# Kernel tuning notes

Hardware: AMD Instinct MI355X
Metric: run time of the kernel (lower is better)

## Reference

```python
import jax, jax.numpy as jnp
import numpy as np

HIDDEN, MSG, KEY, ROUNDS = 256, 64, 16, 2
LN_EPS = 1e-5


def _orthogonal(key, shape, gain):
    # mimic torch orthogonal_ init (exact values don't matter for correctness testing)
    a = jax.random.normal(key, shape, dtype=jnp.float32)
    q, r = jnp.linalg.qr(a.T if shape[0] < shape[1] else a)
    q = q * jnp.sign(jnp.diag(r))
    if shape[0] < shape[1]:
        q = q.T
    return gain * q[:shape[0], :shape[1]]


def setup_inputs() -> dict:
    key = jax.random.key(0)
    ks = jax.random.split(key, 6)
    g = float(np.sqrt(2.0))
    N = 8192
    return {
        "hidden_states": jax.random.normal(ks[0], (N, HIDDEN), dtype=jnp.float32),
        "W_msg": _orthogonal(ks[1], (MSG, HIDDEN), g),
        "b_msg": jnp.zeros((MSG,), jnp.float32),
        "W_key": _orthogonal(ks[2], (KEY, HIDDEN), g),
        "b_key": jnp.zeros((KEY,), jnp.float32),
        "W_qry": _orthogonal(ks[3], (KEY, HIDDEN), g),
        "b_qry": jnp.zeros((KEY,), jnp.float32),
        "W_agg": _orthogonal(ks[4], (HIDDEN, HIDDEN + MSG), g),
        "b_agg": jnp.zeros((HIDDEN,), jnp.float32),
        "ln_g": jnp.ones((HIDDEN,), jnp.float32),
        "ln_b": jnp.zeros((HIDDEN,), jnp.float32),
    }


def reference(hidden_states, W_msg, b_msg, W_key, b_key, W_qry, b_qry,
              W_agg, b_agg, ln_g, ln_b):
    inv_sqrt_k = 1.0 / np.sqrt(KEY)
    h = hidden_states
    attn = None
    for _ in range(ROUNDS):
        msgs = h @ W_msg.T + b_msg          # (N, MSG)
        keys = h @ W_key.T + b_key          # (N, KEY)
        qrys = h @ W_qry.T + b_qry          # (N, KEY)
        scores = (qrys @ keys.T) * inv_sqrt_k  # (N, N)
        attn = jax.nn.softmax(scores, axis=-1)
        agg_msg = attn @ msgs               # (N, MSG)
        combined = jnp.concatenate([h, agg_msg], axis=-1)  # (N, HIDDEN+MSG)
        z = combined @ W_agg.T + b_agg      # (N, HIDDEN)
        mu = jnp.mean(z, axis=-1, keepdims=True)
        var = jnp.mean(jnp.square(z - mu), axis=-1, keepdims=True)
        h = jax.nn.relu(ln_g * (z - mu) * jax.lax.rsqrt(var + LN_EPS) + ln_b)
    return h, attn
```

## Files before the change

kernel.cpp:

```cpp
#include <hip/hip_runtime.h>

constexpr int H = 256, MSGC = 64;
constexpr float LN_EPS = 1e-5f;
constexpr float QSCALE = 0.25f * 1.4426950408889634f;

typedef __attribute__((ext_vector_type(8))) short bf16x8;
typedef __attribute__((ext_vector_type(4))) float f32x4;

__device__ inline ushort f2bf(float x) {
    union { float f; unsigned u; } v; v.f = x;
    unsigned r = v.u + 0x7fffu + ((v.u >> 16) & 1u);
    return (ushort)(r >> 16);
}
__device__ inline float bf2f(ushort h) {
    union { unsigned u; float f; } v; v.u = ((unsigned)h) << 16;
    return v.f;
}
__device__ inline bf16x8 pack_bf16x8(float4 f0, float4 f1) {
    union { unsigned u[4]; bf16x8 v; } cv;
    asm("v_cvt_pk_bf16_f32 %0, %1, %2" : "=v"(cv.u[0]) : "v"(f0.x), "v"(f0.y));
    asm("v_cvt_pk_bf16_f32 %0, %1, %2" : "=v"(cv.u[1]) : "v"(f0.z), "v"(f0.w));
    asm("v_cvt_pk_bf16_f32 %0, %1, %2" : "=v"(cv.u[2]) : "v"(f1.x), "v"(f1.y));
    asm("v_cvt_pk_bf16_f32 %0, %1, %2" : "=v"(cv.u[3]) : "v"(f1.z), "v"(f1.w));
    return cv.v;
}

__global__ __launch_bounds__(256) void prep_kernel(
    const float* __restrict__ Wm, const float* __restrict__ Wk,
    const float* __restrict__ Wq, const float* __restrict__ Wa,
    ushort* __restrict__ Wph, ushort* __restrict__ Wpl,
    ushort* __restrict__ Wfh, ushort* __restrict__ Wfl)
{
    const int t = threadIdx.x, b = blockIdx.x;
    if (b < 48) {
        const int tile = b >> 3, kc = b & 7;
#pragma unroll
        for (int j2 = 0; j2 < 2; ++j2) {
            const int idx = t * 2 + j2;
            const int l = idx >> 3, e = idx & 7;
            const int col = tile * 16 + (l & 15);
            const int k = kc * 32 + (l >> 4) * 8 + e;
            float v;
            if (col < 64)      v = Wm[(size_t)col * H + k];
            else if (col < 80) v = Wk[(size_t)(col - 64) * H + k];
            else               v = QSCALE * Wq[(size_t)(col - 80) * H + k];
            ushort hi = f2bf(v);
            Wph[(size_t)b * 512 + idx] = hi;
            Wpl[(size_t)b * 512 + idx] = f2bf(v - bf2f(hi));
        }
    } else {
        const int unit = b - 48;
        const int ctg = unit / 10, kc = unit % 10;
#pragma unroll
        for (int j2 = 0; j2 < 2; ++j2) {
            const int idx = t * 2 + j2;
            const int l = idx >> 3, e = idx & 7;
            const int col = ctg * 16 + (l & 15);
            const int k = kc * 32 + (l >> 4) * 8 + e;
            const float v = Wa[(size_t)col * 320 + k];
            ushort hi = f2bf(v);
            Wfh[(size_t)unit * 512 + idx] = hi;
            Wfl[(size_t)unit * 512 + idx] = f2bf(v - bf2f(hi));
        }
    }
}

__global__ __launch_bounds__(128) void proj_kernel(
    const float* __restrict__ h,
    const ushort* __restrict__ Wph, const ushort* __restrict__ Wpl,
    const float* __restrict__ bm, const float* __restrict__ bk, const float* __restrict__ bq,
    ushort* __restrict__ msgsF, ushort* __restrict__ kh, ushort* __restrict__ kl,
    ushort* __restrict__ qh, ushort* __restrict__ ql, int n)
{
    constexpr int AST = 264;
    __shared__ ushort Ahi[16 * AST];
    __shared__ ushort Alo[16 * AST];
    const int t = threadIdx.x, lane = t & 63, w = t >> 6;
    const int gq = lane >> 4, c = lane & 15;
    const int r0 = blockIdx.x * 16;
    const float4* hsrc = (const float4*)(h + (size_t)r0 * H);
#pragma unroll
    for (int u = 0; u < 8; ++u) {
        const int idx = t + 128 * u;
        const int row = idx >> 6, c4 = idx & 63;
        float4 v = hsrc[idx];
        ushort4 hi, lo;
        hi.x = f2bf(v.x); lo.x = f2bf(v.x - bf2f(hi.x));
        hi.y = f2bf(v.y); lo.y = f2bf(v.y - bf2f(hi.y));
        hi.z = f2bf(v.z); lo.z = f2bf(v.z - bf2f(hi.z));
        hi.w = f2bf(v.w); lo.w = f2bf(v.w - bf2f(hi.w));
        *(ushort4*)&Ahi[row * AST + c4 * 4] = hi;
        *(ushort4*)&Alo[row * AST + c4 * 4] = lo;
    }
    __syncthreads();
    f32x4 acc[3] = {{0,0,0,0},{0,0,0,0},{0,0,0,0}};
    for (int kc = 0; kc < 8; ++kc) {
        const bf16x8 afh = *(const bf16x8*)&Ahi[c * AST + kc * 32 + gq * 8];
        const bf16x8 afl = *(const bf16x8*)&Alo[c * AST + kc * 32 + gq * 8];
#pragma unroll
        for (int ct = 0; ct < 3; ++ct) {
            const int unit = (w * 3 + ct) * 8 + kc;
            const bf16x8 whi = *(const bf16x8*)(Wph + (size_t)unit * 512 + lane * 8);
            const bf16x8 wlo = *(const bf16x8*)(Wpl + (size_t)unit * 512 + lane * 8);
            acc[ct] = __builtin_amdgcn_mfma_f32_16x16x32_bf16(afh, whi, acc[ct], 0, 0, 0);
            acc[ct] = __builtin_amdgcn_mfma_f32_16x16x32_bf16(afh, wlo, acc[ct], 0, 0, 0);
            acc[ct] = __builtin_amdgcn_mfma_f32_16x16x32_bf16(afl, whi, acc[ct], 0, 0, 0);
        }
    }
#pragma unroll
    for (int ct = 0; ct < 3; ++ct) {
        const int tile = w * 3 + ct;
        if (tile < 4) {
            const float bb = bm[tile * 16 + c];
#pragma unroll
            for (int r = 0; r < 4; ++r) {
                const int j = r0 + gq * 4 + r;
                const size_t idx = ((size_t)(j >> 5) * 4 + tile) * 512
                                 + ((j >> 3) & 3) * 128 + c * 8 + (j & 7);
                msgsF[idx] = f2bf(acc[ct][r] + bb);
            }
        } else if (tile == 4) {
            const float bb = bk[c];
#pragma unroll
            for (int r = 0; r < 4; ++r) {
                const int j = r0 + gq * 4 + r;
                const float v = acc[ct][r] + bb;
                const ushort hi = f2bf(v);
                kh[(size_t)j * 16 + c] = hi;
                kl[(size_t)j * 16 + c] = f2bf(v - bf2f(hi));
            }
        } else {
            const float bb = QSCALE * bq[c];
#pragma unroll
            for (int r = 0; r < 4; ++r) {
                const int j = r0 + gq * 4 + r;
                const float v = acc[ct][r] + bb;
                const ushort hi = f2bf(v);
                qh[(size_t)j * 16 + c] = hi;
                ql[(size_t)j * 16 + c] = f2bf(v - bf2f(hi));
            }
        }
    }
}

__device__ __forceinline__ void loadK(bf16x8* dst, const ushort* __restrict__ kh,
                                      int j0, int g, int c) {
#pragma unroll
    for (int js = 0; js < 4; ++js)
        dst[js] = *(const bf16x8*)(kh + (size_t)(j0 + js * 16 + c) * 16 + 8 * (g & 1));
}

__device__ __forceinline__ void qk_tile(const bf16x8* b1s, const ushort* __restrict__ kl,
                                        int j0, int g, int c, bf16x8 a1, bf16x8 a2,
                                        const bf16x8 zer, f32x4* pd) {
    const f32x4 z4 = {0.f, 0.f, 0.f, 0.f};
    bf16x8 b2s[4];
#pragma unroll
    for (int js = 0; js < 4; ++js)
        b2s[js] = (g < 2) ? *(const bf16x8*)(kl + (size_t)(j0 + js * 16 + c) * 16 + 8 * g) : zer;
#pragma unroll
    for (int js = 0; js < 4; ++js) {
        pd[js] = __builtin_amdgcn_mfma_f32_16x16x32_bf16(a1, b1s[js], z4, 0, 0, 0);
        pd[js] = __builtin_amdgcn_mfma_f32_16x16x32_bf16(a2, b2s[js], pd[js], 0, 0, 0);
    }
}

__device__ __forceinline__ void pv_tile(const float* __restrict__ P,
                                        const ushort* __restrict__ msgsF,
                                        int j0, int g, int c, int w, int lane, f32x4* accv) {
#pragma unroll
    for (int ks = 0; ks < 2; ++ks) {
        const int arow = w * 16 + c;
        const int sw = (arow & 7) << 2;
        const int colb = ks * 32 + 8 * g;
        float4 f0 = *(const float4*)&P[arow * 64 + ((colb) ^ sw)];
        float4 f1 = *(const float4*)&P[arow * 64 + ((colb + 4) ^ sw)];
        bf16x8 af = pack_bf16x8(f0, f1);
        const size_t mbase = ((size_t)(j0 >> 5) + ks) * 4;
#pragma unroll
        for (int mt = 0; mt < 4; ++mt) {
            bf16x8 bfr = *((const bf16x8*)(msgsF + (mbase + mt) * 512) + lane);
            accv[mt] = __builtin_amdgcn_mfma_f32_16x16x32_bf16(af, bfr, accv[mt], 0, 0, 0);
        }
    }
}

__device__ __forceinline__ void expstore(const f32x4* pd, float* Pbuf, float* l,
                                         int w, int g, int c) {
#pragma unroll
    for (int js = 0; js < 4; ++js)
#pragma unroll
        for (int r = 0; r < 4; ++r) {
            const int row = w * 16 + g * 4 + r;
            const float pp = exp2f(pd[js][r]);
            l[r] += pp;
            Pbuf[row * 64 + ((js * 16 + c) ^ ((row & 7) << 2))] = pp;
        }
}

__device__ __forceinline__ void expstore_n(const f32x4* pd, float* Pbuf, const float* rinv,
                                           int w, int g, int c) {
#pragma unroll
    for (int js = 0; js < 4; ++js)
#pragma unroll
        for (int r = 0; r < 4; ++r) {
            const int row = w * 16 + g * 4 + r;
            const float pp = exp2f(pd[js][r]) * rinv[r];
            Pbuf[row * 64 + ((js * 16 + c) ^ ((row & 7) << 2))] = pp;
        }
}

__device__ __forceinline__ void attn_write(const float* __restrict__ Pbuf,
                                           float* __restrict__ attn,
                                           int i0, int j0, int n, int lane, int w) {
    const int c4 = lane & 15;
#pragma unroll
    for (int u = 0; u < 4; ++u) {
        const int row = w * 16 + u * 4 + (lane >> 4);
        const int sw = (row & 7) << 2;
        float4 v = *(const float4*)&Pbuf[row * 64 + ((c4 * 4) ^ sw)];
        *(float4*)(attn + (size_t)(i0 + row) * n + j0 + c4 * 4) = v;
    }
}

__global__ __launch_bounds__(256, 4) void flash1_kernel(
    const ushort* __restrict__ qh, const ushort* __restrict__ ql,
    const ushort* __restrict__ kh, const ushort* __restrict__ kl,
    const ushort* __restrict__ msgsF,
    float* __restrict__ aggO, float* __restrict__ aggL, int n)
{
    __shared__ float P0[64 * 64];
    __shared__ float P1[64 * 64];
    const int t = threadIdx.x, lane = t & 63, w = t >> 6;
    const int g = lane >> 4, c = lane & 15;
    const int i0 = blockIdx.x * 64;
    bf16x8 zer = {0,0,0,0,0,0,0,0};
    f32x4 z4 = {0.f, 0.f, 0.f, 0.f};
    const ushort* qsrc = (g < 2) ? qh : ql;
    bf16x8 a1 = *(const bf16x8*)(qsrc + (size_t)(i0 + w * 16 + c) * 16 + 8 * (g & 1));
    bf16x8 a2 = (g < 2) ? a1 : zer;
    float l[4] = {0.f, 0.f, 0.f, 0.f};
    f32x4 accv[4] = {z4, z4, z4, z4};
    const int nj = n / 8, jb = blockIdx.y * nj;
    bf16x8 bA[4], bB[4];
    loadK(bA, kh, jb, g, c);
    loadK(bB, kh, jb + 64, g, c);
    {
        f32x4 pd[4];
        qk_tile(bA, kl, jb, g, c, a1, a2, zer, pd);
        expstore(pd, P0, l, w, g, c);
    }
    loadK(bA, kh, jb + 128, g, c);
    {
        f32x4 pd[4];
        qk_tile(bB, kl, jb + 64, g, c, a1, a2, zer, pd);
        pv_tile(P0, msgsF, jb, g, c, w, lane, accv);
        expstore(pd, P1, l, w, g, c);
    }
    for (int p = 1; p < 8; ++p) {
        const int tA = jb + p * 128, tB = tA + 64;
        loadK(bB, kh, tB, g, c);
        {
            f32x4 pd[4];
            qk_tile(bA, kl, tA, g, c, a1, a2, zer, pd);
            pv_tile(P1, msgsF, tA - 64, g, c, w, lane, accv);
            expstore(pd, P0, l, w, g, c);
        }
        loadK(bA, kh, (p < 7) ? tA + 128 : tB, g, c);
        {
            f32x4 pd[4];
            qk_tile(bB, kl, tB, g, c, a1, a2, zer, pd);
            pv_tile(P0, msgsF, tA, g, c, w, lane, accv);
            expstore(pd, P1, l, w, g, c);
        }
    }
    pv_tile(P1, msgsF, jb + nj - 64, g, c, w, lane, accv);
#pragma unroll
    for (int r = 0; r < 4; ++r)
#pragma unroll
        for (int d2 = 1; d2 < 16; d2 <<= 1) l[r] += __shfl_xor(l[r], d2, 64);
#pragma unroll
    for (int mt = 0; mt < 4; ++mt)
#pragma unroll
        for (int r = 0; r < 4; ++r)
            aggO[((size_t)blockIdx.y * n + i0 + w * 16 + g * 4 + r) * MSGC + mt * 16 + c] = accv[mt][r];
    if (c == 0) {
#pragma unroll
        for (int r = 0; r < 4; ++r)
            aggL[(size_t)blockIdx.y * n + i0 + w * 16 + g * 4 + r] = l[r];
    }
}

__global__ __launch_bounds__(256, 4) void stats_kernel(
    const ushort* __restrict__ qh, const ushort* __restrict__ ql,
    const ushort* __restrict__ kh, const ushort* __restrict__ kl,
    float* __restrict__ rowl_p, int n)
{
    const int t = threadIdx.x, lane = t & 63, w = t >> 6;
    const int g = lane >> 4, c = lane & 15;
    const int iq = blockIdx.x * 64 + w * 16 + c;
    bf16x8 zer = {0,0,0,0,0,0,0,0};
    const ushort* qsrc = (g < 2) ? qh : ql;
    bf16x8 a1 = *(const bf16x8*)(qsrc + (size_t)iq * 16 + 8 * (g & 1));
    bf16x8 a2 = (g < 2) ? a1 : zer;
    const int nj = n / 8, jb = blockIdx.y * nj;
    float l[4] = {0.f, 0.f, 0.f, 0.f};
    bf16x8 bA[4], bB[4];
    loadK(bA, kh, jb, g, c);
    for (int p = 0; p < 8; ++p) {
        const int t0 = jb + p * 128, t1 = t0 + 64;
        const int t2 = (p < 7) ? t0 + 128 : t1;
        loadK(bB, kh, t1, g, c);
        {
            f32x4 pd[4];
            qk_tile(bA, kl, t0, g, c, a1, a2, zer, pd);
#pragma unroll
            for (int js = 0; js < 4; ++js)
#pragma unroll
                for (int r = 0; r < 4; ++r) l[r] += exp2f(pd[js][r]);
        }
        loadK(bA, kh, t2, g, c);
        {
            f32x4 pd[4];
            qk_tile(bB, kl, t1, g, c, a1, a2, zer, pd);
#pragma unroll
            for (int js = 0; js < 4; ++js)
#pragma unroll
                for (int r = 0; r < 4; ++r) l[r] += exp2f(pd[js][r]);
        }
    }
#pragma unroll
    for (int r = 0; r < 4; ++r)
#pragma unroll
        for (int d2 = 1; d2 < 16; d2 <<= 1) l[r] += __shfl_xor(l[r], d2, 64);
    if (c == 0) {
        const int q0 = blockIdx.x * 64 + w * 16 + g * 4;
#pragma unroll
        for (int r = 0; r < 4; ++r)
            rowl_p[(size_t)blockIdx.y * n + q0 + r] = l[r];
    }
}

__global__ __launch_bounds__(256, 4) void pass2_kernel(
    const ushort* __restrict__ qh, const ushort* __restrict__ ql,
    const ushort* __restrict__ kh, const ushort* __restrict__ kl,
    const ushort* __restrict__ msgsF, const float* __restrict__ rowl_p,
    float* __restrict__ aggO, float* __restrict__ attn, int n)
{
    __shared__ float P0[64 * 64];
    __shared__ float P1[64 * 64];
    const int t = threadIdx.x, lane = t & 63, w = t >> 6;
    const int g = lane >> 4, c = lane & 15;
    const int i0 = blockIdx.x * 64;
    bf16x8 zer = {0,0,0,0,0,0,0,0};
    f32x4 z4 = {0.f, 0.f, 0.f, 0.f};
    const ushort* qsrc = (g < 2) ? qh : ql;
    bf16x8 a1 = *(const bf16x8*)(qsrc + (size_t)(i0 + w * 16 + c) * 16 + 8 * (g & 1));
    bf16x8 a2 = (g < 2) ? a1 : zer;
    float rinv[4];
#pragma unroll
    for (int r = 0; r < 4; ++r) {
        const int q = i0 + w * 16 + g * 4 + r;
        float L = 0.f;
#pragma unroll
        for (int p = 0; p < 8; ++p) L += rowl_p[(size_t)p * n + q];
        rinv[r] = 1.f / L;
    }
    f32x4 accv[4] = {z4, z4, z4, z4};
    const int nj = n / 8, jb = blockIdx.y * nj;
    bf16x8 bA[4], bB[4];
    loadK(bA, kh, jb, g, c);
    loadK(bB, kh, jb + 64, g, c);
    {
        f32x4 pd[4];
        qk_tile(bA, kl, jb, g, c, a1, a2, zer, pd);
        expstore_n(pd, P0, rinv, w, g, c);
    }
    loadK(bA, kh, jb + 128, g, c);
    {
        f32x4 pd[4];
        qk_tile(bB, kl, jb + 64, g, c, a1, a2, zer, pd);
        attn_write(P0, attn, i0, jb, n, lane, w);
        pv_tile(P0, msgsF, jb, g, c, w, lane, accv);
        expstore_n(pd, P1, rinv, w, g, c);
    }
    for (int p = 1; p < 8; ++p) {
        const int tA = jb + p * 128, tB = tA + 64;
        loadK(bB, kh, tB, g, c);
        {
            f32x4 pd[4];
            qk_tile(bA, kl, tA, g, c, a1, a2, zer, pd);
            attn_write(P1, attn, i0, tA - 64, n, lane, w);
            pv_tile(P1, msgsF, tA - 64, g, c, w, lane, accv);
            expstore_n(pd, P0, rinv, w, g, c);
        }
        loadK(bA, kh, (p < 7) ? tA + 128 : tB, g, c);
        {
            f32x4 pd[4];
            qk_tile(bB, kl, tB, g, c, a1, a2, zer, pd);
            attn_write(P0, attn, i0, tA, n, lane, w);
            pv_tile(P0, msgsF, tA, g, c, w, lane, accv);
            expstore_n(pd, P1, rinv, w, g, c);
        }
    }
    attn_write(P1, attn, i0, jb + nj - 64, n, lane, w);
    pv_tile(P1, msgsF, jb + nj - 64, g, c, w, lane, accv);
#pragma unroll
    for (int mt = 0; mt < 4; ++mt)
#pragma unroll
        for (int r = 0; r < 4; ++r) {
            const int row = w * 16 + g * 4 + r;
            aggO[((size_t)blockIdx.y * n + i0 + row) * MSGC + mt * 16 + c] = accv[mt][r];
        }
}

template <bool FLASH>
__global__ __launch_bounds__(256) void aggln_kernel(
    const float* __restrict__ h, const float* __restrict__ aggO,
    const float* __restrict__ aggL,
    const ushort* __restrict__ Wfh, const ushort* __restrict__ Wfl,
    const float* __restrict__ ba,
    const float* __restrict__ gg, const float* __restrict__ bb,
    float* __restrict__ hout, int n)
{
    constexpr int AST = 328;
    __shared__ ushort Ahi[16 * AST];
    __shared__ ushort Alo[16 * AST];
    __shared__ float Linv[16];
    __shared__ float red1[16][4], red2[16][4];
    const int t = threadIdx.x, lane = t & 63, w = t >> 6;
    const int gq = lane >> 4, c = lane & 15;
    const int r0 = blockIdx.x * 16;
    const float4* hsrc = (const float4*)(h + (size_t)r0 * H);
#pragma unroll
    for (int u = 0; u < 4; ++u) {
        const int idx = t + 256 * u;
        const int row = idx >> 6, c4 = idx & 63;
        float4 v = hsrc[idx];
        ushort4 hi, lo;
        hi.x = f2bf(v.x); lo.x = f2bf(v.x - bf2f(hi.x));
        hi.y = f2bf(v.y); lo.y = f2bf(v.y - bf2f(hi.y));
        hi.z = f2bf(v.z); lo.z = f2bf(v.z - bf2f(hi.z));
        hi.w = f2bf(v.w); lo.w = f2bf(v.w - bf2f(hi.w));
        *(ushort4*)&Ahi[row * AST + c4 * 4] = hi;
        *(ushort4*)&Alo[row * AST + c4 * 4] = lo;
    }
    if (FLASH && t < 16) {
        float L = 0.f;
#pragma unroll
        for (int p = 0; p < 8; ++p) L += aggL[(size_t)p * n + r0 + t];
        Linv[t] = 1.f / L;
    }
    __syncthreads();
    {
        const int row = t >> 4, c4 = t & 15;
        float4 s = {0.f, 0.f, 0.f, 0.f};
#pragma unroll
        for (int p = 0; p < 8; ++p) {
            const float4 v = *(const float4*)(aggO + (size_t)p * n * MSGC
                               + (size_t)(r0 + row) * MSGC + c4 * 4);
            s.x += v.x; s.y += v.y; s.z += v.z; s.w += v.w;
        }
        if (FLASH) { const float li = Linv[row]; s.x *= li; s.y *= li; s.z *= li; s.w *= li; }
        ushort4 hi, lo;
        hi.x = f2bf(s.x); lo.x = f2bf(s.x - bf2f(hi.x));
        hi.y = f2bf(s.y); lo.y = f2bf(s.y - bf2f(hi.y));
        hi.z = f2bf(s.z); lo.z = f2bf(s.z - bf2f(hi.z));
        hi.w = f2bf(s.w); lo.w = f2bf(s.w - bf2f(hi.w));
        *(ushort4*)&Ahi[row * AST + 256 + c4 * 4] = hi;
        *(ushort4*)&Alo[row * AST + 256 + c4 * 4] = lo;
    }
    __syncthreads();
    f32x4 acc[4] = {{0,0,0,0},{0,0,0,0},{0,0,0,0},{0,0,0,0}};
    for (int kc = 0; kc < 10; ++kc) {
        const bf16x8 afh = *(const bf16x8*)&Ahi[c * AST + kc * 32 + gq * 8];
        const bf16x8 afl = *(const bf16x8*)&Alo[c * AST + kc * 32 + gq * 8];
#pragma unroll
        for (int ct = 0; ct < 4; ++ct) {
            const int ctg = w * 4 + ct;
            const bf16x8 whi = *(const bf16x8*)(Wfh + ((size_t)(ctg * 10 + kc)) * 512 + lane * 8);
            const bf16x8 wlo = *(const bf16x8*)(Wfl + ((size_t)(ctg * 10 + kc)) * 512 + lane * 8);
            acc[ct] = __builtin_amdgcn_mfma_f32_16x16x32_bf16(afh, whi, acc[ct], 0, 0, 0);
            acc[ct] = __builtin_amdgcn_mfma_f32_16x16x32_bf16(afh, wlo, acc[ct], 0, 0, 0);
            acc[ct] = __builtin_amdgcn_mfma_f32_16x16x32_bf16(afl, whi, acc[ct], 0, 0, 0);
        }
    }
    float bav[4], gv[4], bv[4];
#pragma unroll
    for (int ct = 0; ct < 4; ++ct) {
        const int col = w * 64 + ct * 16 + c;
        bav[ct] = ba[col]; gv[ct] = gg[col]; bv[ct] = bb[col];
    }
#pragma unroll
    for (int ct = 0; ct < 4; ++ct) {
        acc[ct][0] += bav[ct]; acc[ct][1] += bav[ct];
        acc[ct][2] += bav[ct]; acc[ct][3] += bav[ct];
    }
#pragma unroll
    for (int r = 0; r < 4; ++r) {
        float s1 = 0.f, s2 = 0.f;
#pragma unroll
        for (int ct = 0; ct < 4; ++ct) { const float v = acc[ct][r]; s1 += v; s2 += v * v; }
#pragma unroll
        for (int d = 1; d < 16; d <<= 1) { s1 += __shfl_xor(s1, d, 64); s2 += __shfl_xor(s2, d, 64); }
        if (c == 0) { red1[gq * 4 + r][w] = s1; red2[gq * 4 + r][w] = s2; }
    }
    __syncthreads();
#pragma unroll
    for (int r = 0; r < 4; ++r) {
        const int row = gq * 4 + r;
        const float s1 = red1[row][0] + red1[row][1] + red1[row][2] + red1[row][3];
        const float s2 = red2[row][0] + red2[row][1] + red2[row][2] + red2[row][3];
        const float mu = s1 * (1.f / 256.f);
        const float var = s2 * (1.f / 256.f) - mu * mu;
        const float rs = rsqrtf(var + LN_EPS);
#pragma unroll
        for (int ct = 0; ct < 4; ++ct) {
            float o = (acc[ct][r] - mu) * rs * gv[ct] + bv[ct];
            hout[(size_t)(r0 + row) * H + w * 64 + ct * 16 + c] = fmaxf(o, 0.f);
        }
    }
}

extern "C" void kernel_launch(void* const* d_in, const int* in_sizes, int n_in,
                              void* d_out, int out_size, void* d_ws, size_t ws_size,
                              hipStream_t stream)
{
    const float* hs = (const float*)d_in[0];
    const float* Wm = (const float*)d_in[1];
    const float* bm = (const float*)d_in[2];
    const float* Wk = (const float*)d_in[3];
    const float* bk = (const float*)d_in[4];
    const float* Wq = (const float*)d_in[5];
    const float* bq = (const float*)d_in[6];
    const float* Wa = (const float*)d_in[7];
    const float* ba = (const float*)d_in[8];
    const float* lg = (const float*)d_in[9];
    const float* lb = (const float*)d_in[10];
    const int n = in_sizes[0] / H;

    char* wp = (char*)d_ws;
    auto alloc = [&](size_t bytes) { void* p = (void*)wp; wp += (bytes + 255) & ~(size_t)255; return p; };
    float*  h2     = (float*)alloc((size_t)n * H * 4);
    ushort* qh     = (ushort*)alloc((size_t)n * 16 * 2);
    ushort* ql     = (ushort*)alloc((size_t)n * 16 * 2);
    ushort* kh     = (ushort*)alloc((size_t)n * 16 * 2);
    ushort* kl     = (ushort*)alloc((size_t)n * 16 * 2);
    ushort* msgsF  = (ushort*)alloc((size_t)MSGC * n * 2);
    float*  rowl_p = (float*)alloc((size_t)8 * n * 4);
    float*  aggO   = (float*)alloc((size_t)8 * n * MSGC * 4);
    float*  aggL   = (float*)alloc((size_t)8 * n * 4);
    ushort* Wph    = (ushort*)alloc((size_t)48 * 512 * 2);
    ushort* Wpl    = (ushort*)alloc((size_t)48 * 512 * 2);
    ushort* Wfh    = (ushort*)alloc((size_t)160 * 512 * 2);
    ushort* Wfl    = (ushort*)alloc((size_t)160 * 512 * 2);

    float* hOut = (float*)d_out;
    float* attn = hOut + (size_t)n * H;

    prep_kernel<<<208, 256, 0, stream>>>(Wm, Wk, Wq, Wa, Wph, Wpl, Wfh, Wfl);

    proj_kernel<<<n / 16, 128, 0, stream>>>(hs, Wph, Wpl, bm, bk, bq, msgsF, kh, kl, qh, ql, n);
    flash1_kernel<<<dim3(n / 64, 8), 256, 0, stream>>>(qh, ql, kh, kl, msgsF,
                                                       aggO, aggL, n);
    aggln_kernel<true><<<n / 16, 256, 0, stream>>>(hs, aggO, aggL, Wfh, Wfl,
                                                   ba, lg, lb, h2, n);
    proj_kernel<<<n / 16, 128, 0, stream>>>(h2, Wph, Wpl, bm, bk, bq, msgsF, kh, kl, qh, ql, n);
    stats_kernel<<<dim3(n / 64, 8), 256, 0, stream>>>(qh, ql, kh, kl, rowl_p, n);
    pass2_kernel<<<dim3(n / 64, 8), 256, 0, stream>>>(qh, ql, kh, kl, msgsF,
                                                      rowl_p, aggO, attn, n);
    aggln_kernel<false><<<n / 16, 256, 0, stream>>>(h2, aggO, aggL, Wfh, Wfl,
                                                    ba, lg, lb, hOut, n);
}
```

Before: 244.5 us.

## Use native exp2, MFMA priority hints, higher occupancy bounds, 8-row aggln blocks

```diff
diff --git a/kernel.cpp b/kernel.cpp
--- a/kernel.cpp
+++ b/kernel.cpp
@@ -6,6 +6,12 @@
 
 typedef __attribute__((ext_vector_type(8))) short bf16x8;
 typedef __attribute__((ext_vector_type(4))) float f32x4;
+
+#if __has_builtin(__builtin_amdgcn_exp2f)
+__device__ __forceinline__ float fexp2(float x) { return __builtin_amdgcn_exp2f(x); }
+#else
+__device__ __forceinline__ float fexp2(float x) { return exp2f(x); }
+#endif
 
 __device__ inline ushort f2bf(float x) {
     union { float f; unsigned u; } v; v.f = x;
@@ -16,12 +22,17 @@
     union { unsigned u; float f; } v; v.u = ((unsigned)h) << 16;
     return v.f;
 }
+__device__ inline unsigned cvt_pk_u32(float a, float b) {
+    unsigned r;
+    asm("v_cvt_pk_bf16_f32 %0, %1, %2" : "=v"(r) : "v"(a), "v"(b));
+    return r;
+}
 __device__ inline bf16x8 pack_bf16x8(float4 f0, float4 f1) {
     union { unsigned u[4]; bf16x8 v; } cv;
-    asm("v_cvt_pk_bf16_f32 %0, %1, %2" : "=v"(cv.u[0]) : "v"(f0.x), "v"(f0.y));
-    asm("v_cvt_pk_bf16_f32 %0, %1, %2" : "=v"(cv.u[1]) : "v"(f0.z), "v"(f0.w));
-    asm("v_cvt_pk_bf16_f32 %0, %1, %2" : "=v"(cv.u[2]) : "v"(f1.x), "v"(f1.y));
-    asm("v_cvt_pk_bf16_f32 %0, %1, %2" : "=v"(cv.u[3]) : "v"(f1.z), "v"(f1.w));
+    cv.u[0] = cvt_pk_u32(f0.x, f0.y);
+    cv.u[1] = cvt_pk_u32(f0.z, f0.w);
+    cv.u[2] = cvt_pk_u32(f1.x, f1.y);
+    cv.u[3] = cvt_pk_u32(f1.z, f1.w);
     return cv.v;
 }
 
@@ -158,11 +169,13 @@
 #pragma unroll
     for (int js = 0; js < 4; ++js)
         b2s[js] = (g < 2) ? *(const bf16x8*)(kl + (size_t)(j0 + js * 16 + c) * 16 + 8 * g) : zer;
+    __builtin_amdgcn_s_setprio(1);
 #pragma unroll
     for (int js = 0; js < 4; ++js) {
         pd[js] = __builtin_amdgcn_mfma_f32_16x16x32_bf16(a1, b1s[js], z4, 0, 0, 0);
         pd[js] = __builtin_amdgcn_mfma_f32_16x16x32_bf16(a2, b2s[js], pd[js], 0, 0, 0);
     }
+    __builtin_amdgcn_s_setprio(0);
 }
 
 __device__ __forceinline__ void pv_tile(const float* __restrict__ P,
@@ -177,11 +190,13 @@
         float4 f1 = *(const float4*)&P[arow * 64 + ((colb + 4) ^ sw)];
         bf16x8 af = pack_bf16x8(f0, f1);
         const size_t mbase = ((size_t)(j0 >> 5) + ks) * 4;
+        __builtin_amdgcn_s_setprio(1);
 #pragma unroll
         for (int mt = 0; mt < 4; ++mt) {
             bf16x8 bfr = *((const bf16x8*)(msgsF + (mbase + mt) * 512) + lane);
             accv[mt] = __builtin_amdgcn_mfma_f32_16x16x32_bf16(af, bfr, accv[mt], 0, 0, 0);
         }
+        __builtin_amdgcn_s_setprio(0);
     }
 }
 
@@ -192,7 +207,7 @@
 #pragma unroll
         for (int r = 0; r < 4; ++r) {
             const int row = w * 16 + g * 4 + r;
-            const float pp = exp2f(pd[js][r]);
+            const float pp = fexp2(pd[js][r]);
             l[r] += pp;
             Pbuf[row * 64 + ((js * 16 + c) ^ ((row & 7) << 2))] = pp;
         }
@@ -205,14 +220,14 @@
 #pragma unroll
         for (int r = 0; r < 4; ++r) {
             const int row = w * 16 + g * 4 + r;
-            const float pp = exp2f(pd[js][r]) * rinv[r];
+            const float pp = fexp2(pd[js][r]) * rinv[r];
             Pbuf[row * 64 + ((js * 16 + c) ^ ((row & 7) << 2))] = pp;
         }
 }
 
-__device__ __forceinline__ void attn_write(const float* __restrict__ Pbuf,
-                                           float* __restrict__ attn,
-                                           int i0, int j0, int n, int lane, int w) {
+__device__ __forceinline__ void attn_write4(const float* __restrict__ Pbuf,
+                                            float* __restrict__ attn,
+                                            int i0, int j0, int n, int lane, int w) {
     const int c4 = lane & 15;
 #pragma unroll
     for (int u = 0; u < 4; ++u) {
@@ -223,7 +238,7 @@
     }
 }
 
-__global__ __launch_bounds__(256, 4) void flash1_kernel(
+__global__ __launch_bounds__(256, 5) void flash1_kernel(
     const ushort* __restrict__ qh, const ushort* __restrict__ ql,
     const ushort* __restrict__ kh, const ushort* __restrict__ kl,
     const ushort* __restrict__ msgsF,
@@ -291,7 +306,7 @@
     }
 }
 
-__global__ __launch_bounds__(256, 4) void stats_kernel(
+__global__ __launch_bounds__(256, 6) void stats_kernel(
     const ushort* __restrict__ qh, const ushort* __restrict__ ql,
     const ushort* __restrict__ kh, const ushort* __restrict__ kl,
     float* __restrict__ rowl_p, int n)
@@ -317,7 +332,7 @@
 #pragma unroll
             for (int js = 0; js < 4; ++js)
 #pragma unroll
-                for (int r = 0; r < 4; ++r) l[r] += exp2f(pd[js][r]);
+                for (int r = 0; r < 4; ++r) l[r] += fexp2(pd[js][r]);
         }
         loadK(bA, kh, t2, g, c);
         {
@@ -326,7 +341,7 @@
 #pragma unroll
             for (int js = 0; js < 4; ++js)
 #pragma unroll
-                for (int r = 0; r < 4; ++r) l[r] += exp2f(pd[js][r]);
+                for (int r = 0; r < 4; ++r) l[r] += fexp2(pd[js][r]);
         }
     }
 #pragma unroll
@@ -341,7 +356,7 @@
     }
 }
 
-__global__ __launch_bounds__(256, 4) void pass2_kernel(
+__global__ __launch_bounds__(256, 5) void pass2_kernel(
     const ushort* __restrict__ qh, const ushort* __restrict__ ql,
     const ushort* __restrict__ kh, const ushort* __restrict__ kl,
     const ushort* __restrict__ msgsF, const float* __restrict__ rowl_p,
@@ -380,7 +395,7 @@
     {
         f32x4 pd[4];
         qk_tile(bB, kl, jb + 64, g, c, a1, a2, zer, pd);
-        attn_write(P0, attn, i0, jb, n, lane, w);
+        attn_write4(P0, attn, i0, jb, n, lane, w);
         pv_tile(P0, msgsF, jb, g, c, w, lane, accv);
         expstore_n(pd, P1, rinv, w, g, c);
     }
@@ -390,7 +405,7 @@
         {
             f32x4 pd[4];
             qk_tile(bA, kl, tA, g, c, a1, a2, zer, pd);
-            attn_write(P1, attn, i0, tA - 64, n, lane, w);
+            attn_write4(P1, attn, i0, tA - 64, n, lane, w);
             pv_tile(P1, msgsF, tA - 64, g, c, w, lane, accv);
             expstore_n(pd, P0, rinv, w, g, c);
         }
@@ -398,12 +413,12 @@
         {
             f32x4 pd[4];
             qk_tile(bB, kl, tB, g, c, a1, a2, zer, pd);
-            attn_write(P0, attn, i0, tA, n, lane, w);
+            attn_write4(P0, attn, i0, tA, n, lane, w);
             pv_tile(P0, msgsF, tA, g, c, w, lane, accv);
             expstore_n(pd, P1, rinv, w, g, c);
         }
     }
-    attn_write(P1, attn, i0, jb + nj - 64, n, lane, w);
+    attn_write4(P1, attn, i0, jb + nj - 64, n, lane, w);
     pv_tile(P1, msgsF, jb + nj - 64, g, c, w, lane, accv);
 #pragma unroll
     for (int mt = 0; mt < 4; ++mt)
@@ -426,17 +441,17 @@
     constexpr int AST = 328;
     __shared__ ushort Ahi[16 * AST];
     __shared__ ushort Alo[16 * AST];
-    __shared__ float Linv[16];
+    __shared__ float Linv[8];
     __shared__ float red1[16][4], red2[16][4];
     const int t = threadIdx.x, lane = t & 63, w = t >> 6;
     const int gq = lane >> 4, c = lane & 15;
-    const int r0 = blockIdx.x * 16;
+    const int r0 = blockIdx.x * 8;
     const float4* hsrc = (const float4*)(h + (size_t)r0 * H);
 #pragma unroll
     for (int u = 0; u < 4; ++u) {
         const int idx = t + 256 * u;
         const int row = idx >> 6, c4 = idx & 63;
-        float4 v = hsrc[idx];
+        float4 v = (row < 8) ? hsrc[idx] : make_float4(0.f, 0.f, 0.f, 0.f);
         ushort4 hi, lo;
         hi.x = f2bf(v.x); lo.x = f2bf(v.x - bf2f(hi.x));
         hi.y = f2bf(v.y); lo.y = f2bf(v.y - bf2f(hi.y));
@@ -445,14 +460,14 @@
         *(ushort4*)&Ahi[row * AST + c4 * 4] = hi;
         *(ushort4*)&Alo[row * AST + c4 * 4] = lo;
     }
-    if (FLASH && t < 16) {
+    if (FLASH && t < 8) {
         float L = 0.f;
 #pragma unroll
         for (int p = 0; p < 8; ++p) L += aggL[(size_t)p * n + r0 + t];
         Linv[t] = 1.f / L;
     }
     __syncthreads();
-    {
+    if (t < 128) {
         const int row = t >> 4, c4 = t & 15;
         float4 s = {0.f, 0.f, 0.f, 0.f};
 #pragma unroll
@@ -469,6 +484,11 @@
         hi.w = f2bf(s.w); lo.w = f2bf(s.w - bf2f(hi.w));
         *(ushort4*)&Ahi[row * AST + 256 + c4 * 4] = hi;
         *(ushort4*)&Alo[row * AST + 256 + c4 * 4] = lo;
+    } else {
+        const int row = 8 + ((t - 128) >> 4), c4 = (t - 128) & 15;
+        const ushort4 zz = {0, 0, 0, 0};
+        *(ushort4*)&Ahi[row * AST + 256 + c4 * 4] = zz;
+        *(ushort4*)&Alo[row * AST + 256 + c4 * 4] = zz;
     }
     __syncthreads();
     f32x4 acc[4] = {{0,0,0,0},{0,0,0,0},{0,0,0,0},{0,0,0,0}};
@@ -506,18 +526,20 @@
         if (c == 0) { red1[gq * 4 + r][w] = s1; red2[gq * 4 + r][w] = s2; }
     }
     __syncthreads();
-#pragma unroll
-    for (int r = 0; r < 4; ++r) {
-        const int row = gq * 4 + r;
-        const float s1 = red1[row][0] + red1[row][1] + red1[row][2] + red1[row][3];
-        const float s2 = red2[row][0] + red2[row][1] + red2[row][2] + red2[row][3];
-        const float mu = s1 * (1.f / 256.f);
-        const float var = s2 * (1.f / 256.f) - mu * mu;
-        const float rs = rsqrtf(var + LN_EPS);
-#pragma unroll
-        for (int ct = 0; ct < 4; ++ct) {
-            float o = (acc[ct][r] - mu) * rs * gv[ct] + bv[ct];
-            hout[(size_t)(r0 + row) * H + w * 64 + ct * 16 + c] = fmaxf(o, 0.f);
+    if (gq < 2) {
+#pragma unroll
+        for (int r = 0; r < 4; ++r) {
+            const int row = gq * 4 + r;
+            const float s1 = red1[row][0] + red1[row][1] + red1[row][2] + red1[row][3];
+            const float s2 = red2[row][0] + red2[row][1] + red2[row][2] + red2[row][3];
+            const float mu = s1 * (1.f / 256.f);
+            const float var = s2 * (1.f / 256.f) - mu * mu;
+            const float rs = rsqrtf(var + LN_EPS);
+#pragma unroll
+            for (int ct = 0; ct < 4; ++ct) {
+                float o = (acc[ct][r] - mu) * rs * gv[ct] + bv[ct];
+                hout[(size_t)(r0 + row) * H + w * 64 + ct * 16 + c] = fmaxf(o, 0.f);
+            }
         }
     }
 }
@@ -563,12 +585,12 @@
     proj_kernel<<<n / 16, 128, 0, stream>>>(hs, Wph, Wpl, bm, bk, bq, msgsF, kh, kl, qh, ql, n);
     flash1_kernel<<<dim3(n / 64, 8), 256, 0, stream>>>(qh, ql, kh, kl, msgsF,
                                                        aggO, aggL, n);
-    aggln_kernel<true><<<n / 16, 256, 0, stream>>>(hs, aggO, aggL, Wfh, Wfl,
-                                                   ba, lg, lb, h2, n);
+    aggln_kernel<true><<<n / 8, 256, 0, stream>>>(hs, aggO, aggL, Wfh, Wfl,
+                                                  ba, lg, lb, h2, n);
     proj_kernel<<<n / 16, 128, 0, stream>>>(h2, Wph, Wpl, bm, bk, bq, msgsF, kh, kl, qh, ql, n);
     stats_kernel<<<dim3(n / 64, 8), 256, 0, stream>>>(qh, ql, kh, kl, rowl_p, n);
     pass2_kernel<<<dim3(n / 64, 8), 256, 0, stream>>>(qh, ql, kh, kl, msgsF,
                                                       rowl_p, aggO, attn, n);
-    aggln_kernel<false><<<n / 16, 256, 0, stream>>>(h2, aggO, aggL, Wfh, Wfl,
-                                                    ba, lg, lb, hOut, n);
-}
+    aggln_kernel<false><<<n / 8, 256, 0, stream>>>(h2, aggO, aggL, Wfh, Wfl,
+                                                   ba, lg, lb, hOut, n);
+}
```

Result: slower. 444.8 us (+81.9%).
